# Kernel tuning notes

Measured on AMD Instinct MI355X. Metric: run time of the kernel, lower is better.

## Reference

```python
import jax, jax.numpy as jnp
import numpy as np

LEFT, RIGHT, BOTTOM, TOP = -0.5, 0.5, -0.5, 0.5
MIN_BW = MIN_BH = MIN_D = 1e-3
B, CIN, Hh, Ww = 16, 8, 256, 256
C_NN = CIN // 2
C_CO = CIN - C_NN
HID = 64
FT_C = 2


def conv2d(x, w, b, pad):
    y = jax.lax.conv_general_dilated(x, w, (1, 1), [(pad, pad), (pad, pad)],
                                     dimension_numbers=('NCHW', 'OIHW', 'NCHW'))
    return y + b[None, :, None, None]


def f_net(z, w0, b0, w1, b1, w2, b2, w3, b3, w4, b4, wz, bz, logs):
    h = jax.nn.relu(conv2d(z, w0, b0, 1))
    for wi, bi in ((w1, b1), (w2, b2), (w3, b3), (w4, b4)):
        h = jax.nn.relu(conv2d(h, wi, bi, 0))
    h = conv2d(h, wz, bz, 1)
    return h * jnp.exp(3.0 * logs)[None, :, None, None]


def rq_spline_fwd(x, w, h, d):
    # x: [B,C2,H,W]; w,h,d: [B,C2,H,W,1] (NUM_BINS=1 -> spline has 2 bins)
    inside = (x > LEFT) & (x < RIGHT)
    xs = jnp.where(inside, x, 0.0)  # safe value inside the domain
    width = jax.nn.sigmoid(w) * (1.0 - 2.0 * MIN_BW) + MIN_BW
    widths = jnp.concatenate([width, 1.0 - width], -1)
    cw = jnp.cumsum(widths, -1)
    cw = jnp.concatenate([jnp.zeros_like(cw[..., :1]), cw], -1)
    cw = (RIGHT - LEFT) * cw + LEFT
    cw = cw.at[..., 0].set(LEFT).at[..., -1].set(RIGHT)
    widths = cw[..., 1:] - cw[..., :-1]
    derivs = jnp.exp(d) * (1.0 - MIN_D) + MIN_D
    ones = jnp.ones_like(derivs[..., :1])
    derivs = jnp.concatenate([ones, derivs, ones], -1)  # boundary derivs = 1
    hh = jax.nn.sigmoid(h) * (1.0 - 2.0 * MIN_BH) + MIN_BH
    heights = jnp.concatenate([hh, 1.0 - hh], -1)
    ch = jnp.cumsum(heights, -1)
    ch = jnp.concatenate([jnp.zeros_like(ch[..., :1]), ch], -1)
    ch = (TOP - BOTTOM) * ch + BOTTOM
    ch = ch.at[..., 0].set(BOTTOM).at[..., -1].set(TOP)
    heights = ch[..., 1:] - ch[..., :-1]
    # searchsorted with eps bump on last knot
    cw_s = cw.at[..., -1].add(1e-6)
    idx = jnp.clip(jnp.sum((xs[..., None] >= cw_s).astype(jnp.int32), -1) - 1, 0, 1)[..., None]
    g = lambda t: jnp.take_along_axis(t, idx, axis=-1)[..., 0]
    in_cw, in_w = g(cw), g(widths)
    in_ch, in_h = g(ch), g(heights)
    in_delta = g(heights / widths)
    d0, d1 = g(derivs), g(derivs[..., 1:])
    theta = (xs - in_cw) / in_w
    t1mt = theta * (1.0 - theta)
    denom = in_delta + (d0 + d1 - 2.0 * in_delta) * t1mt
    out = in_ch + in_h * (in_delta * theta * theta + d0 * t1mt) / denom
    dnum = in_delta * in_delta * (d1 * theta * theta + 2.0 * in_delta * t1mt + d0 * (1.0 - theta) ** 2)
    lad = jnp.log(dnum) - 2.0 * jnp.log(denom)
    out = jnp.clip(out, BOTTOM, TOP)
    return jnp.where(inside, out, x), jnp.where(inside, lad, 0.0)


def setup_inputs():
    key = jax.random.key(0)
    ks = jax.random.split(key, 8)

    def w_init(k, shape):
        fan_in = shape[1] * shape[2] * shape[3]
        return jax.random.normal(k, shape, jnp.float32) / np.float32(np.sqrt(fan_in))

    return {
        'input': jax.random.normal(ks[0], (B, CIN, Hh, Ww), jnp.float32) * 0.5,
        'logdet': jnp.zeros((B,), jnp.float32),
        'ft': jax.random.normal(ks[1], (B, FT_C, Hh, Ww), jnp.float32),
        'w0': w_init(ks[2], (HID, C_NN + FT_C, 3, 3)), 'b0': jnp.zeros((HID,), jnp.float32),
        'w1': w_init(ks[3], (HID, HID, 1, 1)), 'b1': jnp.zeros((HID,), jnp.float32),
        'w2': w_init(ks[4], (HID, HID, 1, 1)), 'b2': jnp.zeros((HID,), jnp.float32),
        'w3': w_init(ks[5], (HID, HID, 1, 1)), 'b3': jnp.zeros((HID,), jnp.float32),
        'w4': w_init(ks[6], (HID, HID, 1, 1)), 'b4': jnp.zeros((HID,), jnp.float32),
        'wz': w_init(ks[7], (C_CO * 4, HID, 3, 3)) * 0.1, 'bz': jnp.zeros((C_CO * 4,), jnp.float32),
        'logs': jnp.zeros((C_CO * 4,), jnp.float32),
    }


def reference(input, logdet, ft, w0, b0, w1, b1, w2, b2, w3, b3, w4, b4, wz, bz, logs):
    z1, z2 = input[:, :C_NN], input[:, C_NN:]
    hfeat = f_net(jnp.concatenate([z1, ft], axis=1), w0, b0, w1, b1, w2, b2, w3, b3, w4, b4, wz, bz, logs)
    # [B, C_co*4, H, W] -> [B, C_co, H, W, 4]: width | height | derivative | shift
    newh = hfeat.reshape(B, C_CO, 4, Hh, Ww).transpose(0, 1, 3, 4, 2)
    width, height, deriv, shift = newh[..., 0:1], newh[..., 1:2], newh[..., 2:3], newh[..., 3]
    out2, lad = rq_spline_fwd(z2, width, height, deriv)
    out2 = out2 + shift
    output = jnp.concatenate([z1, out2], axis=1)
    return output, logdet + jnp.sum(lad, axis=(1, 2, 3))
```

## Files before the change

### kernel.cpp

```cpp
#include <hip/hip_runtime.h>
#include <math.h>

#define OUT_TAIL (16*8*256*256)
#define HSTR   68
#define HROWB  136
#define SSTRIDE 2176
#define INSTR  408

typedef __bf16 bf8_t __attribute__((ext_vector_type(8)));
typedef float  f4_t  __attribute__((ext_vector_type(4)));

__device__ __forceinline__ unsigned rne16u_(float x) {
    unsigned u = __float_as_uint(x);
    return (u + 0x7fffu + ((u >> 16) & 1u)) >> 16;
}
#if __has_builtin(__builtin_amdgcn_cvt_pk_bf16_f32)
__device__ __forceinline__ unsigned pack2f(float a, float b) {
    typedef __bf16 bf2_t __attribute__((ext_vector_type(2)));
    bf2_t r = __builtin_amdgcn_cvt_pk_bf16_f32(a, b);
    return __builtin_bit_cast(unsigned, r);
}
#else
__device__ __forceinline__ unsigned pack2f(float a, float b) {
    unsigned r;
    asm("v_cvt_pk_bf16_f32 %0, %1, %2" : "=v"(r) : "v"(a), "v"(b));
    return r;
}
#endif
__device__ __forceinline__ bf8_t as_bf8(uint4 u) { return __builtin_bit_cast(bf8_t, u); }

__global__ void prep_kernel(const float* __restrict__ w0, const float* __restrict__ w1,
                            const float* __restrict__ w2, const float* __restrict__ w3,
                            const float* __restrict__ w4, const float* __restrict__ wz,
                            unsigned int* __restrict__ ws) {
    int f = blockIdx.x;
    int lane = threadIdx.x;
    int m = lane & 15, qd = lane >> 4;
    float vals[8];
    if (f < 8) {
        int Mt = f >> 1, ks = f & 1;
        int c = Mt * 16 + m;
        for (int j = 0; j < 8; ++j) {
            int k = ks * 32 + qd * 8 + j;
            vals[j] = (k < 54) ? w0[c * 54 + k] : 0.0f;
        }
    } else if (f < 40) {
        int r = f - 8, l = r >> 3, fr = r & 7;
        int Mt = fr >> 1, ks = fr & 1;
        const float* wp = (l == 0) ? w1 : (l == 1) ? w2 : (l == 2) ? w3 : w4;
        int c = Mt * 16 + m;
        for (int j = 0; j < 8; ++j) vals[j] = wp[c * 64 + ks * 32 + qd * 8 + j];
    } else {
        int r = f - 40, tap = r >> 1, ks = r & 1;
        for (int j = 0; j < 8; ++j) {
            int k = ks * 32 + qd * 8 + j;
            vals[j] = wz[(m * 64 + k) * 9 + tap];
        }
    }
    unsigned int hi[4], lo[4];
    for (int i = 0; i < 4; ++i) {
        float a = vals[2 * i], c = vals[2 * i + 1];
        unsigned ha = rne16u_(a), hc = rne16u_(c);
        float ra = a - __uint_as_float(ha << 16);
        float rc = c - __uint_as_float(hc << 16);
        hi[i] = ha | (hc << 16);
        lo[i] = rne16u_(ra) | (rne16u_(rc) << 16);
    }
    unsigned int* p = ws + (size_t)(f * 64 + lane) * 8;
    for (int i = 0; i < 4; ++i) { p[i] = hi[i]; p[4 + i] = lo[i]; }
}

__global__ void init_logdet_kernel(const float* __restrict__ logdet, float* __restrict__ outp) {
    int i = threadIdx.x;
    if (i < 16) outp[OUT_TAIL + i] = logdet[i];
}

__global__ __launch_bounds__(256, 3)
void fused_kernel(const float* __restrict__ input, const float* __restrict__ ft,
                  const float* __restrict__ b0, const float* __restrict__ b1,
                  const float* __restrict__ b2, const float* __restrict__ b3,
                  const float* __restrict__ b4, const float* __restrict__ bz,
                  const float* __restrict__ logs, const unsigned int* __restrict__ wsp,
                  float* __restrict__ outp)
{
    __shared__ __align__(16) unsigned short Hs[336 * HSTR];
    __shared__ __align__(16) unsigned short in_s[2464];
    __shared__ float red[4];

    const int tid = threadIdx.x;
    const int bx = blockIdx.x, by = blockIdx.y, b = blockIdx.z;
    const int lane = tid & 63;
    const int ws_ = __builtin_amdgcn_readfirstlane(tid >> 6);
    const int m = lane & 15, q = lane >> 4;
    const uint4* W4 = (const uint4*)wsp;
    const bool border = (bx == 0) | (bx == 15) | (by == 0) | (by == 15);

    {
        const int x0 = bx * 16 - 2, y0 = by * 16 - 2;
        int yy1 = tid / 20, xx1 = tid - yy1 * 20;
        int t2 = tid + 256;
        int yy2 = t2 / 20, xx2 = t2 - yy2 * 20;
        int gy1 = y0 + yy1, gx1 = x0 + xx1;
        int gy2 = y0 + yy2, gx2 = x0 + xx2;
        bool ok1 = ((unsigned)gy1 < 256u) && ((unsigned)gx1 < 256u);
        bool ok2 = ((unsigned)gy2 < 256u) && ((unsigned)gx2 < 256u);
        #pragma unroll
        for (int c = 0; c < 6; ++c) {
            const float* src = (c < 4) ? input + (size_t)(b * 8 + c) * 65536
                                       : ft + (size_t)(b * 2 + (c - 4)) * 65536;
            float v1 = ok1 ? src[gy1 * 256 + gx1] : 0.0f;
            in_s[c * INSTR + yy1 * 20 + xx1] = (unsigned short)(pack2f(v1, 0.0f) & 0xffffu);
            if (tid < 144) {
                float v2 = ok2 ? src[gy2 * 256 + gx2] : 0.0f;
                in_s[c * INSTR + yy2 * 20 + xx2] = (unsigned short)(pack2f(v2, 0.0f) & 0xffffu);
            }
        }
        int c = tid >> 6;
        int rem = (tid & 63) * 4;
        int oy = rem >> 4, ox = rem & 15;
        size_t o = ((size_t)(b * 8 + c) * 256 + by * 16 + oy) * 256 + bx * 16 + ox;
        *(float4*)&outp[o] = *(const float4*)&input[o];
    }
    __syncthreads();

    const int nstrip = (ws_ == 0) ? 6 : 5;
    const int pbase  = (ws_ == 0) ? 0 : (80 * ws_ + 16);
    const int pix0   = pbase + m;
    const int A0 = pix0 * HROWB + q * 16;
    const int W0 = pix0 * HROWB + q * 8;

    {
        int koffB[16];
        #pragma unroll
        for (int ks = 0; ks < 2; ++ks)
            #pragma unroll
            for (int j = 0; j < 8; ++j) {
                int k = ks * 32 + q * 8 + j;
                int ch = k / 9, tap = k - ch * 9;
                int ky = tap / 3, kx = tap - ky * 3;
                koffB[ks * 8 + j] = (k < 54) ? (ch * INSTR + ky * 20 + kx) * 2 : 0;
            }
        uint4 Ah[8];
        #pragma unroll
        for (int f = 0; f < 8; ++f)
            Ah[f] = W4[((size_t)(f * 64) + lane) * 2];
        f4_t bv4[4];
        #pragma unroll
        for (int Mt = 0; Mt < 4; ++Mt)
            #pragma unroll
            for (int r = 0; r < 4; ++r) bv4[Mt][r] = b0[Mt * 16 + q * 4 + r];

        int cpy = (pix0 * 1821) >> 15;
        int cpx = pix0 - cpy * 18;
        #pragma unroll
        for (int s = 0; s < 6; ++s) {
            if (s < nstrip) {
                int ib = (cpy * 20 + cpx) * 2;
                unsigned e[16];
                #pragma unroll
                for (int i = 0; i < 16; ++i)
                    e[i] = *(const unsigned short*)((const char*)in_s + ib + koffB[i]);
                uint4 B0 = make_uint4(e[0] | (e[1] << 16), e[2] | (e[3] << 16),
                                      e[4] | (e[5] << 16), e[6] | (e[7] << 16));
                uint4 B1 = make_uint4(e[8] | (e[9] << 16), e[10] | (e[11] << 16),
                                      e[12] | (e[13] << 16), e[14] | (e[15] << 16));
                #pragma unroll
                for (int Mt = 0; Mt < 4; ++Mt) {
                    f4_t a = __builtin_amdgcn_mfma_f32_16x16x32_bf16(as_bf8(Ah[Mt*2+0]), as_bf8(B0), bv4[Mt], 0, 0, 0);
                    a = __builtin_amdgcn_mfma_f32_16x16x32_bf16(as_bf8(Ah[Mt*2+1]), as_bf8(B1), a, 0, 0, 0);
                    uint2 pr;
                    pr.x = pack2f(fmaxf(a[0], 0.f), fmaxf(a[1], 0.f));
                    pr.y = pack2f(fmaxf(a[2], 0.f), fmaxf(a[3], 0.f));
                    *(uint2*)((char*)Hs + W0 + s * SSTRIDE + Mt * 32) = pr;
                }
            }
            cpx += 16;
            if (cpx >= 18) { cpx -= 18; cpy += 1; }
        }
    }

    #pragma unroll 1
    for (int l = 0; l < 4; ++l) {
        const float* bl = (l == 0) ? b1 : (l == 1) ? b2 : (l == 2) ? b3 : b4;
        uint4 Ah[8];
        #pragma unroll
        for (int f = 0; f < 8; ++f)
            Ah[f] = W4[((size_t)((8 + l * 8 + f) * 64) + lane) * 2];
        f4_t bv4[4];
        #pragma unroll
        for (int Mt = 0; Mt < 4; ++Mt)
            #pragma unroll
            for (int r = 0; r < 4; ++r) bv4[Mt][r] = bl[Mt * 16 + q * 4 + r];

        #pragma unroll
        for (int s = 0; s < 6; ++s) {
            if (s < nstrip) {
                const char* rp = (const char*)Hs + A0 + s * SSTRIDE;
                uint2 a0 = *(const uint2*)(rp);
                uint2 a1 = *(const uint2*)(rp + 8);
                uint2 a2 = *(const uint2*)(rp + 64);
                uint2 a3 = *(const uint2*)(rp + 72);
                uint4 B0 = make_uint4(a0.x, a0.y, a1.x, a1.y);
                uint4 B1 = make_uint4(a2.x, a2.y, a3.x, a3.y);
                #pragma unroll
                for (int Mt = 0; Mt < 4; ++Mt) {
                    f4_t a = __builtin_amdgcn_mfma_f32_16x16x32_bf16(as_bf8(Ah[Mt*2+0]), as_bf8(B0), bv4[Mt], 0, 0, 0);
                    a = __builtin_amdgcn_mfma_f32_16x16x32_bf16(as_bf8(Ah[Mt*2+1]), as_bf8(B1), a, 0, 0, 0);
                    uint2 pr;
                    pr.x = pack2f(fmaxf(a[0], 0.f), fmaxf(a[1], 0.f));
                    pr.y = pack2f(fmaxf(a[2], 0.f), fmaxf(a[3], 0.f));
                    *(uint2*)((char*)Hs + W0 + s * SSTRIDE + Mt * 32) = pr;
                }
            }
        }
    }

    if (border) {
        #pragma unroll
        for (int s = 0; s < 6; ++s) {
            if (s < nstrip) {
                int pixs = pix0 + 16 * s;
                int pys = (pixs * 1821) >> 15;
                int pxs = pixs - pys * 18;
                int gy = by * 16 - 1 + pys, gx = bx * 16 - 1 + pxs;
                if (!(((unsigned)gy < 256u) && ((unsigned)gx < 256u))) {
                    char* zp = (char*)Hs + A0 + s * SSTRIDE;
                    *(uint2*)(zp)      = make_uint2(0, 0);
                    *(uint2*)(zp + 8)  = make_uint2(0, 0);
                    *(uint2*)(zp + 64) = make_uint2(0, 0);
                    *(uint2*)(zp + 72) = make_uint2(0, 0);
                }
            }
        }
    }
    __syncthreads();

    {
        float xv[4];
        #pragma unroll
        for (int rr = 0; rr < 4; ++rr) {
            int gy = by * 16 + ws_ * 4 + rr;
            xv[rr] = input[((size_t)(b * 8 + 4 + q) * 256 + gy) * 256 + bx * 16 + m];
        }
        float bzv[4], scl[4];
        #pragma unroll
        for (int r = 0; r < 4; ++r) {
            int c = q * 4 + r;
            bzv[r] = bz[c];
            scl[r] = __expf(3.0f * logs[c]);
        }
        f4_t acc[4];
        #pragma unroll
        for (int rr = 0; rr < 4; ++rr) { acc[rr][0]=0.f; acc[rr][1]=0.f; acc[rr][2]=0.f; acc[rr][3]=0.f; }
        const int Z0 = (ws_ * 72 + m) * HROWB + q * 16;
        #pragma unroll
        for (int tap = 0; tap < 9; ++tap) {
            const int ky = tap / 3, kx = tap - ky * 3;
            #pragma unroll
            for (int ks = 0; ks < 2; ++ks) {
                const uint4* p = W4 + ((size_t)((40 + tap * 2 + ks) * 64) + lane) * 2;
                uint4 ah = p[0], al = p[1];
                #pragma unroll
                for (int rr = 0; rr < 4; ++rr) {
                    const char* zp = (const char*)Hs + Z0 + ((rr + ky) * 18 + kx) * HROWB + ks * 64;
                    uint2 u0 = *(const uint2*)zp;
                    uint2 u1 = *(const uint2*)(zp + 8);
                    uint4 Bv = make_uint4(u0.x, u0.y, u1.x, u1.y);
                    acc[rr] = __builtin_amdgcn_mfma_f32_16x16x32_bf16(as_bf8(ah), as_bf8(Bv), acc[rr], 0, 0, 0);
                    acc[rr] = __builtin_amdgcn_mfma_f32_16x16x32_bf16(as_bf8(al), as_bf8(Bv), acc[rr], 0, 0, 0);
                }
            }
        }
        float lad_sum = 0.0f;
        #pragma unroll
        for (int rr = 0; rr < 4; ++rr) {
            int gy = by * 16 + ws_ * 4 + rr, gx = bx * 16 + m;
            size_t xi = ((size_t)(b * 8 + 4 + q) * 256 + gy) * 256 + gx;
            float x = xv[rr];
            float pw = (acc[rr][0] + bzv[0]) * scl[0];
            float ph = (acc[rr][1] + bzv[1]) * scl[1];
            float pd = (acc[rr][2] + bzv[2]) * scl[2];
            float ps = (acc[rr][3] + bzv[3]) * scl[3];

            bool inside = (x > -0.5f) && (x < 0.5f);
            float xs = inside ? x : 0.0f;
            float wf = 1.0f / (1.0f + __expf(-pw)) * 0.998f + 0.001f;
            float hh = 1.0f / (1.0f + __expf(-ph)) * 0.998f + 0.001f;
            float dd = __expf(pd) * 0.999f + 0.001f;
            bool bin1 = (xs >= wf - 0.5f);
            float in_cw = bin1 ? (wf - 0.5f) : -0.5f;
            float in_w  = bin1 ? (1.0f - wf) : wf;
            float in_ch = bin1 ? (hh - 0.5f) : -0.5f;
            float in_h  = bin1 ? (1.0f - hh) : hh;
            float delta = in_h / in_w;
            float d0 = bin1 ? dd : 1.0f;
            float d1 = bin1 ? 1.0f : dd;
            float theta = (xs - in_cw) / in_w;
            float t1mt  = theta * (1.0f - theta);
            float denom = delta + (d0 + d1 - 2.0f * delta) * t1mt;
            float th2   = theta * theta;
            float ov    = in_ch + in_h * (delta * th2 + d0 * t1mt) / denom;
            float omt   = 1.0f - theta;
            float dnum  = delta * delta * (d1 * th2 + 2.0f * delta * t1mt + d0 * omt * omt);
            float lad   = __logf(dnum) - 2.0f * __logf(denom);
            ov  = fminf(fmaxf(ov, -0.5f), 0.5f);
            ov  = inside ? ov : x;
            lad = inside ? lad : 0.0f;
            outp[xi] = ov + ps;
            lad_sum += lad;
        }
        #pragma unroll
        for (int off = 32; off > 0; off >>= 1)
            lad_sum += __shfl_down(lad_sum, off, 64);
        if (lane == 0) red[ws_] = lad_sum;
    }
    __syncthreads();
    if (tid == 0)
        atomicAdd(&outp[OUT_TAIL + b], red[0] + red[1] + red[2] + red[3]);
}

extern "C" void kernel_launch(void* const* d_in, const int* in_sizes, int n_in,
                              void* d_out, int out_size, void* d_ws, size_t ws_size,
                              hipStream_t stream) {
    const float* input  = (const float*)d_in[0];
    const float* logdet = (const float*)d_in[1];
    const float* ft     = (const float*)d_in[2];
    const float* w0 = (const float*)d_in[3];
    const float* b0 = (const float*)d_in[4];
    const float* w1 = (const float*)d_in[5];
    const float* b1 = (const float*)d_in[6];
    const float* w2 = (const float*)d_in[7];
    const float* b2 = (const float*)d_in[8];
    const float* w3 = (const float*)d_in[9];
    const float* b3 = (const float*)d_in[10];
    const float* w4 = (const float*)d_in[11];
    const float* b4 = (const float*)d_in[12];
    const float* wz = (const float*)d_in[13];
    const float* bz = (const float*)d_in[14];
    const float* logs = (const float*)d_in[15];
    float* outp = (float*)d_out;
    unsigned int* wsp = (unsigned int*)d_ws;

    prep_kernel<<<58, 64, 0, stream>>>(w0, w1, w2, w3, w4, wz, wsp);
    init_logdet_kernel<<<1, 64, 0, stream>>>(logdet, outp);
    fused_kernel<<<dim3(16, 16, 16), 256, 0, stream>>>(
        input, ft, b0, b1, b2, b3, b4, bz, logs, wsp, outp);
}
```

Baseline: 234.3 us.

## Double block size to 512 threads and split strips across eight waves

The fused MLP-conv-spline kernel now runs with 512 threads (8 waves) per block instead of 256. Each wave handles 2-3 strips instead of 5-6 and 2 output rows instead of 4 in the final 3x3 conv and spline stage. The input staging loop and passthrough copy are re-indexed for the larger block. This raises wave-level parallelism per tile so more waves can hide MFMA and LDS latency. The cost is that each wave reloads all the weight fragments for only half the work, and the launch bound of 4 blocks caps registers per thread, which may cause spills.

New measurement: 256.8 us. +9.6%, slower.

```diff
diff --git a/kernel.cpp b/kernel.cpp
--- a/kernel.cpp
+++ b/kernel.cpp
@@ -75,7 +75,7 @@
     if (i < 16) outp[OUT_TAIL + i] = logdet[i];
 }
 
-__global__ __launch_bounds__(256, 3)
+__global__ __launch_bounds__(512, 4)
 void fused_kernel(const float* __restrict__ input, const float* __restrict__ ft,
                   const float* __restrict__ b0, const float* __restrict__ b1,
                   const float* __restrict__ b2, const float* __restrict__ b3,
@@ -85,7 +85,7 @@
 {
     __shared__ __align__(16) unsigned short Hs[336 * HSTR];
     __shared__ __align__(16) unsigned short in_s[2464];
-    __shared__ float red[4];
+    __shared__ float red[8];
 
     const int tid = threadIdx.x;
     const int bx = blockIdx.x, by = blockIdx.y, b = blockIdx.z;
@@ -97,34 +97,26 @@
 
     {
         const int x0 = bx * 16 - 2, y0 = by * 16 - 2;
-        int yy1 = tid / 20, xx1 = tid - yy1 * 20;
-        int t2 = tid + 256;
-        int yy2 = t2 / 20, xx2 = t2 - yy2 * 20;
-        int gy1 = y0 + yy1, gx1 = x0 + xx1;
-        int gy2 = y0 + yy2, gx2 = x0 + xx2;
-        bool ok1 = ((unsigned)gy1 < 256u) && ((unsigned)gx1 < 256u);
-        bool ok2 = ((unsigned)gy2 < 256u) && ((unsigned)gx2 < 256u);
-        #pragma unroll
-        for (int c = 0; c < 6; ++c) {
-            const float* src = (c < 4) ? input + (size_t)(b * 8 + c) * 65536
-                                       : ft + (size_t)(b * 2 + (c - 4)) * 65536;
-            float v1 = ok1 ? src[gy1 * 256 + gx1] : 0.0f;
-            in_s[c * INSTR + yy1 * 20 + xx1] = (unsigned short)(pack2f(v1, 0.0f) & 0xffffu);
-            if (tid < 144) {
-                float v2 = ok2 ? src[gy2 * 256 + gx2] : 0.0f;
-                in_s[c * INSTR + yy2 * 20 + xx2] = (unsigned short)(pack2f(v2, 0.0f) & 0xffffu);
-            }
-        }
-        int c = tid >> 6;
-        int rem = (tid & 63) * 4;
-        int oy = rem >> 4, ox = rem & 15;
+        for (int idx = tid; idx < 2400; idx += 512) {
+            int c = idx / 400, r = idx - c * 400;
+            int yy = r / 20, xx = r - yy * 20;
+            int gy = y0 + yy, gx = x0 + xx;
+            float v = 0.0f;
+            if ((unsigned)gy < 256u && (unsigned)gx < 256u)
+                v = (c < 4) ? input[((size_t)(b * 8 + c) * 256 + gy) * 256 + gx]
+                            : ft[((size_t)(b * 2 + (c - 4)) * 256 + gy) * 256 + gx];
+            in_s[c * INSTR + yy * 20 + xx] = (unsigned short)(pack2f(v, 0.0f) & 0xffffu);
+        }
+        int idx = tid * 2;
+        int c = idx >> 8, q2 = idx & 255;
+        int oy = q2 >> 4, ox = q2 & 15;
         size_t o = ((size_t)(b * 8 + c) * 256 + by * 16 + oy) * 256 + bx * 16 + ox;
-        *(float4*)&outp[o] = *(const float4*)&input[o];
+        *(float2*)&outp[o] = *(const float2*)&input[o];
     }
     __syncthreads();
 
-    const int nstrip = (ws_ == 0) ? 6 : 5;
-    const int pbase  = (ws_ == 0) ? 0 : (80 * ws_ + 16);
+    const int nstrip = (ws_ < 5) ? 3 : 2;
+    const int pbase  = (ws_ < 5) ? (48 * ws_) : (240 + 32 * (ws_ - 5));
     const int pix0   = pbase + m;
     const int A0 = pix0 * HROWB + q * 16;
     const int W0 = pix0 * HROWB + q * 8;
@@ -153,7 +145,7 @@
         int cpy = (pix0 * 1821) >> 15;
         int cpx = pix0 - cpy * 18;
         #pragma unroll
-        for (int s = 0; s < 6; ++s) {
+        for (int s = 0; s < 3; ++s) {
             if (s < nstrip) {
                 int ib = (cpy * 20 + cpx) * 2;
                 unsigned e[16];
@@ -193,7 +185,7 @@
             for (int r = 0; r < 4; ++r) bv4[Mt][r] = bl[Mt * 16 + q * 4 + r];
 
         #pragma unroll
-        for (int s = 0; s < 6; ++s) {
+        for (int s = 0; s < 3; ++s) {
             if (s < nstrip) {
                 const char* rp = (const char*)Hs + A0 + s * SSTRIDE;
                 uint2 a0 = *(const uint2*)(rp);
@@ -217,7 +209,7 @@
 
     if (border) {
         #pragma unroll
-        for (int s = 0; s < 6; ++s) {
+        for (int s = 0; s < 3; ++s) {
             if (s < nstrip) {
                 int pixs = pix0 + 16 * s;
                 int pys = (pixs * 1821) >> 15;
@@ -236,10 +228,10 @@
     __syncthreads();
 
     {
-        float xv[4];
-        #pragma unroll
-        for (int rr = 0; rr < 4; ++rr) {
-            int gy = by * 16 + ws_ * 4 + rr;
+        float xv[2];
+        #pragma unroll
+        for (int rr = 0; rr < 2; ++rr) {
+            int gy = by * 16 + ws_ * 2 + rr;
             xv[rr] = input[((size_t)(b * 8 + 4 + q) * 256 + gy) * 256 + bx * 16 + m];
         }
         float bzv[4], scl[4];
@@ -249,10 +241,10 @@
             bzv[r] = bz[c];
             scl[r] = __expf(3.0f * logs[c]);
         }
-        f4_t acc[4];
-        #pragma unroll
-        for (int rr = 0; rr < 4; ++rr) { acc[rr][0]=0.f; acc[rr][1]=0.f; acc[rr][2]=0.f; acc[rr][3]=0.f; }
-        const int Z0 = (ws_ * 72 + m) * HROWB + q * 16;
+        f4_t acc[2];
+        #pragma unroll
+        for (int rr = 0; rr < 2; ++rr) { acc[rr][0]=0.f; acc[rr][1]=0.f; acc[rr][2]=0.f; acc[rr][3]=0.f; }
+        const int Z0 = (ws_ * 36 + m) * HROWB + q * 16;
         #pragma unroll
         for (int tap = 0; tap < 9; ++tap) {
             const int ky = tap / 3, kx = tap - ky * 3;
@@ -261,7 +253,7 @@
                 const uint4* p = W4 + ((size_t)((40 + tap * 2 + ks) * 64) + lane) * 2;
                 uint4 ah = p[0], al = p[1];
                 #pragma unroll
-                for (int rr = 0; rr < 4; ++rr) {
+                for (int rr = 0; rr < 2; ++rr) {
                     const char* zp = (const char*)Hs + Z0 + ((rr + ky) * 18 + kx) * HROWB + ks * 64;
                     uint2 u0 = *(const uint2*)zp;
                     uint2 u1 = *(const uint2*)(zp + 8);
@@ -273,8 +265,8 @@
         }
         float lad_sum = 0.0f;
         #pragma unroll
-        for (int rr = 0; rr < 4; ++rr) {
-            int gy = by * 16 + ws_ * 4 + rr, gx = bx * 16 + m;
+        for (int rr = 0; rr < 2; ++rr) {
+            int gy = by * 16 + ws_ * 2 + rr, gx = bx * 16 + m;
             size_t xi = ((size_t)(b * 8 + 4 + q) * 256 + gy) * 256 + gx;
             float x = xv[rr];
             float pw = (acc[rr][0] + bzv[0]) * scl[0];
@@ -315,8 +307,12 @@
         if (lane == 0) red[ws_] = lad_sum;
     }
     __syncthreads();
-    if (tid == 0)
-        atomicAdd(&outp[OUT_TAIL + b], red[0] + red[1] + red[2] + red[3]);
+    if (tid == 0) {
+        float t = 0.0f;
+        #pragma unroll
+        for (int i = 0; i < 8; ++i) t += red[i];
+        atomicAdd(&outp[OUT_TAIL + b], t);
+    }
 }
 
 extern "C" void kernel_launch(void* const* d_in, const int* in_sizes, int n_in,
@@ -343,6 +339,6 @@
 
     prep_kernel<<<58, 64, 0, stream>>>(w0, w1, w2, w3, w4, wz, wsp);
     init_logdet_kernel<<<1, 64, 0, stream>>>(logdet, outp);
-    fused_kernel<<<dim3(16, 16, 16), 256, 0, stream>>>(
+    fused_kernel<<<dim3(16, 16, 16), 512, 0, stream>>>(
         input, ft, b0, b1, b2, b3, b4, bz, logs, wsp, outp);
 }
```

## Keep hidden activations in registers across 1x1 layers using 16x16x16 MFMA

Applied to the files above, without the earlier changes.

The four 1x1 conv layers no longer round-trip activations through LDS. The MFMA accumulator output layout of 16x16x16 bf16 matches its B-operand layout, so packed ReLU outputs feed the next layer directly from registers. Weights are re-packed by extra prep blocks into a new workspace region in the matching 4-element fragment layout. This removes LDS writes and reads per layer, but doubles the MFMA instruction count and holds 6x4 uint2 of activations per thread in registers, which may lower occupancy.

After: 237.9 us. Within noise of the previous version (+1.5%).

```diff
diff --git a/kernel.cpp b/kernel.cpp
--- a/kernel.cpp
+++ b/kernel.cpp
@@ -6,6 +6,7 @@
 #define HROWB  136
 #define SSTRIDE 2176
 #define INSTR  408
+#define WS2OFF 29696
 
 typedef __bf16 bf8_t __attribute__((ext_vector_type(8)));
 typedef float  f4_t  __attribute__((ext_vector_type(4)));
@@ -28,6 +29,20 @@
 }
 #endif
 __device__ __forceinline__ bf8_t as_bf8(uint4 u) { return __builtin_bit_cast(bf8_t, u); }
+
+#if __has_builtin(__builtin_amdgcn_mfma_f32_16x16x16_bf16)
+typedef __bf16 bf4_t __attribute__((ext_vector_type(4)));
+__device__ __forceinline__ f4_t mfma16(uint2 a, uint2 b, f4_t c) {
+    return __builtin_amdgcn_mfma_f32_16x16x16_bf16(
+        __builtin_bit_cast(bf4_t, a), __builtin_bit_cast(bf4_t, b), c, 0, 0, 0);
+}
+#else
+typedef short s4_t __attribute__((ext_vector_type(4)));
+__device__ __forceinline__ f4_t mfma16(uint2 a, uint2 b, f4_t c) {
+    return __builtin_amdgcn_mfma_f32_16x16x16bf16_1k(
+        __builtin_bit_cast(s4_t, a), __builtin_bit_cast(s4_t, b), c, 0, 0, 0);
+}
+#endif
 
 __global__ void prep_kernel(const float* __restrict__ w0, const float* __restrict__ w1,
                             const float* __restrict__ w2, const float* __restrict__ w3,
@@ -36,6 +51,20 @@
     int f = blockIdx.x;
     int lane = threadIdx.x;
     int m = lane & 15, qd = lane >> 4;
+    if (f >= 58) {
+        int r = f - 58, l = r >> 4, fr = r & 15;
+        int Mt = fr >> 2, c = fr & 3;
+        const float* wp = (l == 0) ? w1 : (l == 1) ? w2 : (l == 2) ? w3 : w4;
+        int co = Mt * 16 + m;
+        float v0 = wp[co * 64 + c * 16 + qd * 4 + 0];
+        float v1 = wp[co * 64 + c * 16 + qd * 4 + 1];
+        float v2 = wp[co * 64 + c * 16 + qd * 4 + 2];
+        float v3 = wp[co * 64 + c * 16 + qd * 4 + 3];
+        unsigned int* p = ws + WS2OFF + (size_t)((l * 16 + Mt * 4 + c) * 64 + lane) * 2;
+        p[0] = rne16u_(v0) | (rne16u_(v1) << 16);
+        p[1] = rne16u_(v2) | (rne16u_(v3) << 16);
+        return;
+    }
     float vals[8];
     if (f < 8) {
         int Mt = f >> 1, ks = f & 1;
@@ -45,11 +74,7 @@
             vals[j] = (k < 54) ? w0[c * 54 + k] : 0.0f;
         }
     } else if (f < 40) {
-        int r = f - 8, l = r >> 3, fr = r & 7;
-        int Mt = fr >> 1, ks = fr & 1;
-        const float* wp = (l == 0) ? w1 : (l == 1) ? w2 : (l == 2) ? w3 : w4;
-        int c = Mt * 16 + m;
-        for (int j = 0; j < 8; ++j) vals[j] = wp[c * 64 + ks * 32 + qd * 8 + j];
+        for (int j = 0; j < 8; ++j) vals[j] = 0.0f;
     } else {
         int r = f - 40, tap = r >> 1, ks = r & 1;
         for (int j = 0; j < 8; ++j) {
@@ -129,6 +154,8 @@
     const int A0 = pix0 * HROWB + q * 16;
     const int W0 = pix0 * HROWB + q * 8;
 
+    uint2 Bc[6][4];
+
     {
         int koffB[16];
         #pragma unroll
@@ -168,10 +195,8 @@
                 for (int Mt = 0; Mt < 4; ++Mt) {
                     f4_t a = __builtin_amdgcn_mfma_f32_16x16x32_bf16(as_bf8(Ah[Mt*2+0]), as_bf8(B0), bv4[Mt], 0, 0, 0);
                     a = __builtin_amdgcn_mfma_f32_16x16x32_bf16(as_bf8(Ah[Mt*2+1]), as_bf8(B1), a, 0, 0, 0);
-                    uint2 pr;
-                    pr.x = pack2f(fmaxf(a[0], 0.f), fmaxf(a[1], 0.f));
-                    pr.y = pack2f(fmaxf(a[2], 0.f), fmaxf(a[3], 0.f));
-                    *(uint2*)((char*)Hs + W0 + s * SSTRIDE + Mt * 32) = pr;
+                    Bc[s][Mt].x = pack2f(fmaxf(a[0], 0.f), fmaxf(a[1], 0.f));
+                    Bc[s][Mt].y = pack2f(fmaxf(a[2], 0.f), fmaxf(a[3], 0.f));
                 }
             }
             cpx += 16;
@@ -182,10 +207,10 @@
     #pragma unroll 1
     for (int l = 0; l < 4; ++l) {
         const float* bl = (l == 0) ? b1 : (l == 1) ? b2 : (l == 2) ? b3 : b4;
-        uint4 Ah[8];
-        #pragma unroll
-        for (int f = 0; f < 8; ++f)
-            Ah[f] = W4[((size_t)((8 + l * 8 + f) * 64) + lane) * 2];
+        uint2 Aw[16];
+        #pragma unroll
+        for (int f = 0; f < 16; ++f)
+            Aw[f] = *(const uint2*)(wsp + WS2OFF + (size_t)((l * 16 + f) * 64 + lane) * 2);
         f4_t bv4[4];
         #pragma unroll
         for (int Mt = 0; Mt < 4; ++Mt)
@@ -195,26 +220,32 @@
         #pragma unroll
         for (int s = 0; s < 6; ++s) {
             if (s < nstrip) {
-                const char* rp = (const char*)Hs + A0 + s * SSTRIDE;
-                uint2 a0 = *(const uint2*)(rp);
-                uint2 a1 = *(const uint2*)(rp + 8);
-                uint2 a2 = *(const uint2*)(rp + 64);
-                uint2 a3 = *(const uint2*)(rp + 72);
-                uint4 B0 = make_uint4(a0.x, a0.y, a1.x, a1.y);
-                uint4 B1 = make_uint4(a2.x, a2.y, a3.x, a3.y);
+                f4_t acc[4];
                 #pragma unroll
                 for (int Mt = 0; Mt < 4; ++Mt) {
-                    f4_t a = __builtin_amdgcn_mfma_f32_16x16x32_bf16(as_bf8(Ah[Mt*2+0]), as_bf8(B0), bv4[Mt], 0, 0, 0);
-                    a = __builtin_amdgcn_mfma_f32_16x16x32_bf16(as_bf8(Ah[Mt*2+1]), as_bf8(B1), a, 0, 0, 0);
-                    uint2 pr;
-                    pr.x = pack2f(fmaxf(a[0], 0.f), fmaxf(a[1], 0.f));
-                    pr.y = pack2f(fmaxf(a[2], 0.f), fmaxf(a[3], 0.f));
-                    *(uint2*)((char*)Hs + W0 + s * SSTRIDE + Mt * 32) = pr;
-                }
-            }
-        }
-    }
-
+                    f4_t a = bv4[Mt];
+                    #pragma unroll
+                    for (int c = 0; c < 4; ++c)
+                        a = mfma16(Aw[Mt * 4 + c], Bc[s][c], a);
+                    acc[Mt] = a;
+                }
+                #pragma unroll
+                for (int Mt = 0; Mt < 4; ++Mt) {
+                    Bc[s][Mt].x = pack2f(fmaxf(acc[Mt][0], 0.f), fmaxf(acc[Mt][1], 0.f));
+                    Bc[s][Mt].y = pack2f(fmaxf(acc[Mt][2], 0.f), fmaxf(acc[Mt][3], 0.f));
+                }
+            }
+        }
+    }
+
+    #pragma unroll
+    for (int s = 0; s < 6; ++s) {
+        if (s < nstrip) {
+            #pragma unroll
+            for (int Mt = 0; Mt < 4; ++Mt)
+                *(uint2*)((char*)Hs + W0 + s * SSTRIDE + Mt * 32) = Bc[s][Mt];
+        }
+    }
     if (border) {
         #pragma unroll
         for (int s = 0; s < 6; ++s) {
@@ -341,7 +372,7 @@
     float* outp = (float*)d_out;
     unsigned int* wsp = (unsigned int*)d_ws;
 
-    prep_kernel<<<58, 64, 0, stream>>>(w0, w1, w2, w3, w4, wz, wsp);
+    prep_kernel<<<122, 64, 0, stream>>>(w0, w1, w2, w3, w4, wz, wsp);
     init_logdet_kernel<<<1, 64, 0, stream>>>(logdet, outp);
     fused_kernel<<<dim3(16, 16, 16), 256, 0, stream>>>(
         input, ft, b0, b1, b2, b3, b4, bz, logs, wsp, outp);
```

## Software-pipeline weight loads and input gathers across fused conv layers

Applied to the files above, without the earlier changes.

Prefetches the next layer's weight fragments and biases into double-buffered registers while the current layer's MFMAs run, and fully unrolls the layer loop. It also gathers the next strip's first-layer inputs ahead of use and prefetches the final 3x3 conv's per-tap weights one tap ahead. The x, bias and scale loads for the final stage are hoisted above the barrier. The aim is to hide global and LDS load latency behind MFMA work, at the cost of much higher register pressure, which could reduce occupancy or cause spills.

Result: faster. 228.1 us (-2.6%).

```diff
diff --git a/kernel.cpp b/kernel.cpp
--- a/kernel.cpp
+++ b/kernel.cpp
@@ -28,6 +28,9 @@
 }
 #endif
 __device__ __forceinline__ bf8_t as_bf8(uint4 u) { return __builtin_bit_cast(bf8_t, u); }
+__device__ __forceinline__ f4_t mfma32(uint4 a, uint4 b, f4_t c) {
+    return __builtin_amdgcn_mfma_f32_16x16x32_bf16(as_bf8(a), as_bf8(b), c, 0, 0, 0);
+}
 
 __global__ void prep_kernel(const float* __restrict__ w0, const float* __restrict__ w1,
                             const float* __restrict__ w2, const float* __restrict__ w3,
@@ -123,11 +126,26 @@
     }
     __syncthreads();
 
-    const int nstrip = (ws_ == 0) ? 6 : 5;
-    const int pbase  = (ws_ == 0) ? 0 : (80 * ws_ + 16);
-    const int pix0   = pbase + m;
+    const int pbase = (ws_ == 0) ? 0 : (80 * ws_ + 16);
+    const int pix0  = pbase + m;
     const int A0 = pix0 * HROWB + q * 16;
     const int W0 = pix0 * HROWB + q * 8;
+
+    int ibs[6];
+    {
+        int cpy = (pix0 * 1821) >> 15;
+        int cpx = pix0 - cpy * 18;
+        #pragma unroll
+        for (int s = 0; s < 6; ++s) {
+            ibs[s] = (cpy * 20 + cpx) * 2;
+            cpx += 16;
+            if (cpx >= 18) { cpx -= 18; cpy += 1; }
+        }
+    }
+
+    uint4 Aw[2][8];
+    f4_t  bvl[2][4];
+    uint4 czA[2], czL[2];
 
     {
         int koffB[16];
@@ -140,85 +158,129 @@
                 int ky = tap / 3, kx = tap - ky * 3;
                 koffB[ks * 8 + j] = (k < 54) ? (ch * INSTR + ky * 20 + kx) * 2 : 0;
             }
-        uint4 Ah[8];
+        uint4 Ah0[8];
         #pragma unroll
         for (int f = 0; f < 8; ++f)
-            Ah[f] = W4[((size_t)(f * 64) + lane) * 2];
-        f4_t bv4[4];
+            Ah0[f] = W4[((size_t)(f * 64) + lane) * 2];
+        f4_t bc0[4];
         #pragma unroll
         for (int Mt = 0; Mt < 4; ++Mt)
-            #pragma unroll
-            for (int r = 0; r < 4; ++r) bv4[Mt][r] = b0[Mt * 16 + q * 4 + r];
-
-        int cpy = (pix0 * 1821) >> 15;
-        int cpx = pix0 - cpy * 18;
+            bc0[Mt] = *(const f4_t*)(b0 + Mt * 16 + q * 4);
+
+        #define GATHER(ib, B0, B1) {                                            \
+            unsigned e[16];                                                     \
+            _Pragma("unroll")                                                   \
+            for (int i = 0; i < 16; ++i)                                        \
+                e[i] = *(const unsigned short*)((const char*)in_s + (ib) + koffB[i]); \
+            B0 = make_uint4(e[0]|(e[1]<<16), e[2]|(e[3]<<16),                   \
+                            e[4]|(e[5]<<16), e[6]|(e[7]<<16));                  \
+            B1 = make_uint4(e[8]|(e[9]<<16), e[10]|(e[11]<<16),                 \
+                            e[12]|(e[13]<<16), e[14]|(e[15]<<16));              \
+        }
+
+        uint4 Gc0, Gc1, Gn0, Gn1;
+        GATHER(ibs[0], Gc0, Gc1);
+        #pragma unroll
+        for (int s = 0; s < 5; ++s) {
+            if (s == 0) {
+                #pragma unroll
+                for (int f = 0; f < 8; ++f)
+                    Aw[0][f] = W4[((size_t)((8 + f) * 64) + lane) * 2];
+                #pragma unroll
+                for (int Mt = 0; Mt < 4; ++Mt)
+                    bvl[0][Mt] = *(const f4_t*)(b1 + Mt * 16 + q * 4);
+            }
+            if ((s < 4) || (ws_ == 0)) GATHER(ibs[s + 1], Gn0, Gn1);
+            #pragma unroll
+            for (int Mt = 0; Mt < 4; ++Mt) {
+                f4_t a = mfma32(Ah0[2*Mt], Gc0, bc0[Mt]);
+                a = mfma32(Ah0[2*Mt+1], Gc1, a);
+                uint2 pr;
+                pr.x = pack2f(fmaxf(a[0], 0.f), fmaxf(a[1], 0.f));
+                pr.y = pack2f(fmaxf(a[2], 0.f), fmaxf(a[3], 0.f));
+                *(uint2*)((char*)Hs + W0 + s * SSTRIDE + Mt * 32) = pr;
+            }
+            Gc0 = Gn0; Gc1 = Gn1;
+        }
+        if (ws_ == 0) {
+            #pragma unroll
+            for (int Mt = 0; Mt < 4; ++Mt) {
+                f4_t a = mfma32(Ah0[2*Mt], Gc0, bc0[Mt]);
+                a = mfma32(Ah0[2*Mt+1], Gc1, a);
+                uint2 pr;
+                pr.x = pack2f(fmaxf(a[0], 0.f), fmaxf(a[1], 0.f));
+                pr.y = pack2f(fmaxf(a[2], 0.f), fmaxf(a[3], 0.f));
+                *(uint2*)((char*)Hs + W0 + 5 * SSTRIDE + Mt * 32) = pr;
+            }
+        }
+        #undef GATHER
+    }
+
+    #pragma unroll
+    for (int l = 0; l < 4; ++l) {
+        const int cur = l & 1, nxt = cur ^ 1;
+        uint2 Bsl[5][4];
+        #pragma unroll
+        for (int s = 0; s < 5; ++s) {
+            const char* rp = (const char*)Hs + A0 + s * SSTRIDE;
+            Bsl[s][0] = *(const uint2*)(rp);
+            Bsl[s][1] = *(const uint2*)(rp + 8);
+            Bsl[s][2] = *(const uint2*)(rp + 64);
+            Bsl[s][3] = *(const uint2*)(rp + 72);
+        }
+        if (l < 3) {
+            #pragma unroll
+            for (int f = 0; f < 8; ++f)
+                Aw[nxt][f] = W4[((size_t)((8 + (l + 1) * 8 + f) * 64) + lane) * 2];
+            const float* bn = (l == 0) ? b2 : (l == 1) ? b3 : b4;
+            #pragma unroll
+            for (int Mt = 0; Mt < 4; ++Mt)
+                bvl[nxt][Mt] = *(const f4_t*)(bn + Mt * 16 + q * 4);
+        } else {
+            #pragma unroll
+            for (int ks = 0; ks < 2; ++ks) {
+                const uint4* p = W4 + ((size_t)((40 + ks) * 64) + lane) * 2;
+                czA[ks] = p[0]; czL[ks] = p[1];
+            }
+        }
+        #pragma unroll
+        for (int s = 0; s < 5; ++s) {
+            uint4 B0 = make_uint4(Bsl[s][0].x, Bsl[s][0].y, Bsl[s][1].x, Bsl[s][1].y);
+            uint4 B1 = make_uint4(Bsl[s][2].x, Bsl[s][2].y, Bsl[s][3].x, Bsl[s][3].y);
+            #pragma unroll
+            for (int Mt = 0; Mt < 4; ++Mt) {
+                f4_t a = mfma32(Aw[cur][2*Mt], B0, bvl[cur][Mt]);
+                a = mfma32(Aw[cur][2*Mt+1], B1, a);
+                uint2 pr;
+                pr.x = pack2f(fmaxf(a[0], 0.f), fmaxf(a[1], 0.f));
+                pr.y = pack2f(fmaxf(a[2], 0.f), fmaxf(a[3], 0.f));
+                *(uint2*)((char*)Hs + W0 + s * SSTRIDE + Mt * 32) = pr;
+            }
+        }
+        if (ws_ == 0) {
+            const char* rp = (const char*)Hs + A0 + 5 * SSTRIDE;
+            uint2 a0 = *(const uint2*)(rp);
+            uint2 a1 = *(const uint2*)(rp + 8);
+            uint2 a2 = *(const uint2*)(rp + 64);
+            uint2 a3 = *(const uint2*)(rp + 72);
+            uint4 B0 = make_uint4(a0.x, a0.y, a1.x, a1.y);
+            uint4 B1 = make_uint4(a2.x, a2.y, a3.x, a3.y);
+            #pragma unroll
+            for (int Mt = 0; Mt < 4; ++Mt) {
+                f4_t a = mfma32(Aw[cur][2*Mt], B0, bvl[cur][Mt]);
+                a = mfma32(Aw[cur][2*Mt+1], B1, a);
+                uint2 pr;
+                pr.x = pack2f(fmaxf(a[0], 0.f), fmaxf(a[1], 0.f));
+                pr.y = pack2f(fmaxf(a[2], 0.f), fmaxf(a[3], 0.f));
+                *(uint2*)((char*)Hs + W0 + 5 * SSTRIDE + Mt * 32) = pr;
+            }
+        }
+    }
+
+    if (border) {
         #pragma unroll
         for (int s = 0; s < 6; ++s) {
-            if (s < nstrip) {
-                int ib = (cpy * 20 + cpx) * 2;
-                unsigned e[16];
-                #pragma unroll
-                for (int i = 0; i < 16; ++i)
-                    e[i] = *(const unsigned short*)((const char*)in_s + ib + koffB[i]);
-                uint4 B0 = make_uint4(e[0] | (e[1] << 16), e[2] | (e[3] << 16),
-                                      e[4] | (e[5] << 16), e[6] | (e[7] << 16));
-                uint4 B1 = make_uint4(e[8] | (e[9] << 16), e[10] | (e[11] << 16),
-                                      e[12] | (e[13] << 16), e[14] | (e[15] << 16));
-                #pragma unroll
-                for (int Mt = 0; Mt < 4; ++Mt) {
-                    f4_t a = __builtin_amdgcn_mfma_f32_16x16x32_bf16(as_bf8(Ah[Mt*2+0]), as_bf8(B0), bv4[Mt], 0, 0, 0);
-                    a = __builtin_amdgcn_mfma_f32_16x16x32_bf16(as_bf8(Ah[Mt*2+1]), as_bf8(B1), a, 0, 0, 0);
-                    uint2 pr;
-                    pr.x = pack2f(fmaxf(a[0], 0.f), fmaxf(a[1], 0.f));
-                    pr.y = pack2f(fmaxf(a[2], 0.f), fmaxf(a[3], 0.f));
-                    *(uint2*)((char*)Hs + W0 + s * SSTRIDE + Mt * 32) = pr;
-                }
-            }
-            cpx += 16;
-            if (cpx >= 18) { cpx -= 18; cpy += 1; }
-        }
-    }
-
-    #pragma unroll 1
-    for (int l = 0; l < 4; ++l) {
-        const float* bl = (l == 0) ? b1 : (l == 1) ? b2 : (l == 2) ? b3 : b4;
-        uint4 Ah[8];
-        #pragma unroll
-        for (int f = 0; f < 8; ++f)
-            Ah[f] = W4[((size_t)((8 + l * 8 + f) * 64) + lane) * 2];
-        f4_t bv4[4];
-        #pragma unroll
-        for (int Mt = 0; Mt < 4; ++Mt)
-            #pragma unroll
-            for (int r = 0; r < 4; ++r) bv4[Mt][r] = bl[Mt * 16 + q * 4 + r];
-
-        #pragma unroll
-        for (int s = 0; s < 6; ++s) {
-            if (s < nstrip) {
-                const char* rp = (const char*)Hs + A0 + s * SSTRIDE;
-                uint2 a0 = *(const uint2*)(rp);
-                uint2 a1 = *(const uint2*)(rp + 8);
-                uint2 a2 = *(const uint2*)(rp + 64);
-                uint2 a3 = *(const uint2*)(rp + 72);
-                uint4 B0 = make_uint4(a0.x, a0.y, a1.x, a1.y);
-                uint4 B1 = make_uint4(a2.x, a2.y, a3.x, a3.y);
-                #pragma unroll
-                for (int Mt = 0; Mt < 4; ++Mt) {
-                    f4_t a = __builtin_amdgcn_mfma_f32_16x16x32_bf16(as_bf8(Ah[Mt*2+0]), as_bf8(B0), bv4[Mt], 0, 0, 0);
-                    a = __builtin_amdgcn_mfma_f32_16x16x32_bf16(as_bf8(Ah[Mt*2+1]), as_bf8(B1), a, 0, 0, 0);
-                    uint2 pr;
-                    pr.x = pack2f(fmaxf(a[0], 0.f), fmaxf(a[1], 0.f));
-                    pr.y = pack2f(fmaxf(a[2], 0.f), fmaxf(a[3], 0.f));
-                    *(uint2*)((char*)Hs + W0 + s * SSTRIDE + Mt * 32) = pr;
-                }
-            }
-        }
-    }
-
-    if (border) {
-        #pragma unroll
-        for (int s = 0; s < 6; ++s) {
-            if (s < nstrip) {
+            if (s < 5 || ws_ == 0) {
                 int pixs = pix0 + 16 * s;
                 int pys = (pixs * 1821) >> 15;
                 int pxs = pixs - pys * 18;
@@ -233,43 +295,51 @@
             }
         }
     }
+
+    float xv[4], bzv[4], scl[4];
+    #pragma unroll
+    for (int rr = 0; rr < 4; ++rr) {
+        int gy = by * 16 + ws_ * 4 + rr;
+        xv[rr] = input[((size_t)(b * 8 + 4 + q) * 256 + gy) * 256 + bx * 16 + m];
+    }
+    #pragma unroll
+    for (int r = 0; r < 4; ++r) {
+        int c = q * 4 + r;
+        bzv[r] = bz[c];
+        scl[r] = __expf(3.0f * logs[c]);
+    }
     __syncthreads();
 
     {
-        float xv[4];
-        #pragma unroll
-        for (int rr = 0; rr < 4; ++rr) {
-            int gy = by * 16 + ws_ * 4 + rr;
-            xv[rr] = input[((size_t)(b * 8 + 4 + q) * 256 + gy) * 256 + bx * 16 + m];
-        }
-        float bzv[4], scl[4];
-        #pragma unroll
-        for (int r = 0; r < 4; ++r) {
-            int c = q * 4 + r;
-            bzv[r] = bz[c];
-            scl[r] = __expf(3.0f * logs[c]);
-        }
         f4_t acc[4];
         #pragma unroll
         for (int rr = 0; rr < 4; ++rr) { acc[rr][0]=0.f; acc[rr][1]=0.f; acc[rr][2]=0.f; acc[rr][3]=0.f; }
         const int Z0 = (ws_ * 72 + m) * HROWB + q * 16;
         #pragma unroll
         for (int tap = 0; tap < 9; ++tap) {
+            uint4 nA[2], nL[2];
+            if (tap < 8) {
+                #pragma unroll
+                for (int ks = 0; ks < 2; ++ks) {
+                    const uint4* p = W4 + ((size_t)((40 + (tap + 1) * 2 + ks) * 64) + lane) * 2;
+                    nA[ks] = p[0]; nL[ks] = p[1];
+                }
+            }
             const int ky = tap / 3, kx = tap - ky * 3;
             #pragma unroll
             for (int ks = 0; ks < 2; ++ks) {
-                const uint4* p = W4 + ((size_t)((40 + tap * 2 + ks) * 64) + lane) * 2;
-                uint4 ah = p[0], al = p[1];
                 #pragma unroll
                 for (int rr = 0; rr < 4; ++rr) {
                     const char* zp = (const char*)Hs + Z0 + ((rr + ky) * 18 + kx) * HROWB + ks * 64;
                     uint2 u0 = *(const uint2*)zp;
                     uint2 u1 = *(const uint2*)(zp + 8);
                     uint4 Bv = make_uint4(u0.x, u0.y, u1.x, u1.y);
-                    acc[rr] = __builtin_amdgcn_mfma_f32_16x16x32_bf16(as_bf8(ah), as_bf8(Bv), acc[rr], 0, 0, 0);
-                    acc[rr] = __builtin_amdgcn_mfma_f32_16x16x32_bf16(as_bf8(al), as_bf8(Bv), acc[rr], 0, 0, 0);
+                    acc[rr] = mfma32(czA[ks], Bv, acc[rr]);
+                    acc[rr] = mfma32(czL[ks], Bv, acc[rr]);
                 }
             }
+            czA[0] = nA[0]; czA[1] = nA[1];
+            czL[0] = nL[0]; czL[1] = nL[1];
         }
         float lad_sum = 0.0f;
         #pragma unroll
```
